# Kernel optimization log

Hardware: AMD Instinct MI355X
Metric: run time of the kernel (lower is better)

Reference implementation:

```python
import jax, jax.numpy as jnp
import numpy as np

# Constants matching init_kwargs
PC_MIN_X, PC_MIN_Y = -70.4, -40.0
VX, VY = 0.1, 0.1
RADII = (0.4, 0.8)
NSAMPLE = 16
EPS = 1e-5

B, K, N = 2, 2048, 16384
C_BEV, H_BEV, W_BEV = 256, 100, 176


def setup_inputs() -> dict:
    key = jax.random.key(0)
    ks = jax.random.split(key, 16)
    u = lambda k, s: jax.random.uniform(k, s, jnp.float32)
    kp = jnp.stack([
        u(ks[0], (B, K)) * 136.0 - 68.0,
        u(ks[1], (B, K)) * 76.0 - 38.0,
        u(ks[2], (B, K)) * 2.5 - 2.0,   # z in (-2.0, 0.5) -> kpt_mask all True
    ], axis=-1)
    pts = jnp.stack([
        u(ks[3], (B, N)) * 140.0 - 70.0,
        u(ks[4], (B, N)) * 80.0 - 40.0,
        u(ks[5], (B, N)) * 4.0 - 3.0,
    ], axis=-1)
    r = lambda k, s: jax.random.normal(k, s, jnp.float32)
    s01 = lambda k, s: r(k, s) * 0.1
    return {
        "keypoints": kp,
        "points_xyz": pts,
        "points_feat": r(ks[6], (B, N, 1)),
        "spatial_features": r(ks[7], (B, C_BEV, H_BEV, W_BEV)),
        "bev_stride": 8,
        "W0_s0": s01(ks[8], (16, 4)), "g0_s0": jnp.ones(16), "b0_s0": jnp.zeros(16),
        "W1_s0": s01(ks[9], (16, 16)), "g1_s0": jnp.ones(16), "b1_s0": jnp.zeros(16),
        "W0_s1": s01(ks[10], (16, 4)), "g0_s1": jnp.ones(16), "b0_s1": jnp.zeros(16),
        "W1_s1": s01(ks[11], (32, 16)), "g1_s1": jnp.ones(32), "b1_s1": jnp.zeros(32),
        "Wf": s01(ks[12], (128, 304)), "gf": jnp.ones(128), "bf": jnp.zeros(128),
    }


def _batchnorm(x, g, b, axes):
    m = x.mean(axes, keepdims=True)
    v = x.var(axes, keepdims=True)
    return (x - m) * jax.lax.rsqrt(v + EPS) * g + b


def _ball_group(dist2, xyz_b, feat_b, kp_b, radius, ns):
    """pcdet ball_query: first ns in-radius neighbors (index order), pad by first idx."""
    Kq, Np = dist2.shape
    within = dist2 < radius * radius                      # (K, N)
    order = jnp.cumsum(within, axis=1) - 1                # slot for each point
    valid = within & (order < ns)
    pos = jnp.where(valid, order, ns)                     # invalid -> overflow slot
    idx = jnp.zeros((Kq, ns + 1), jnp.int32)
    idx = idx.at[jnp.arange(Kq)[:, None], pos].set(
        jnp.broadcast_to(jnp.arange(Np, dtype=jnp.int32)[None, :], (Kq, Np)))
    idx = idx[:, :ns]
    cnt = within.sum(axis=1)
    slot_ok = jnp.arange(ns)[None, :] < cnt[:, None]
    idx = jnp.where(slot_ok, idx, idx[:, :1])             # replicate first found idx
    empty = cnt == 0
    grouped_xyz = xyz_b[idx] - kp_b[:, None, :]           # (K, ns, 3)
    grouped = jnp.concatenate([grouped_xyz, feat_b[idx]], axis=-1)  # (K, ns, 3+C)
    grouped = jnp.where(empty[:, None, None], 0.0, grouped)
    return grouped, empty


def _group_both_scales(xyz_b, feat_b, kp_b):
    # pairwise dist computed ONCE, shared across both radii
    dist2 = jnp.sum((kp_b[:, None, :] - xyz_b[None, :, :]) ** 2, axis=-1)  # (K, N)
    g0, e0 = _ball_group(dist2, xyz_b, feat_b, kp_b, RADII[0], NSAMPLE)
    g1, e1 = _ball_group(dist2, xyz_b, feat_b, kp_b, RADII[1], NSAMPLE)
    return g0, e0, g1, e1


def _shared_mlp_pool(grouped, empty, layers):
    x = grouped                                            # (B, K, ns, Cin)
    for (W, g, b) in layers:
        x = jnp.einsum('bknc,oc->bkno', x, W)
        x = _batchnorm(x, g, b, axes=(0, 1, 2))            # BN2d over stacked M*ns
        x = jax.nn.relu(x)
    pooled = x.max(axis=2)                                 # max over ns -> (B, K, Cout)
    return jnp.where(empty[:, :, None], 0.0, pooled)


def _bev_interp(bev, kp, stride):
    # bev: (B, C, H, W); kp: (B, K, 3)
    im = jnp.transpose(bev, (0, 2, 3, 1))                  # (B, H, W, C)
    x = (kp[..., 0] - PC_MIN_X) / VX / stride
    y = (kp[..., 1] - PC_MIN_Y) / VY / stride
    Hh, Ww = im.shape[1], im.shape[2]
    x0 = jnp.clip(jnp.floor(x).astype(jnp.int32), 0, Ww - 1)
    x1 = jnp.clip(jnp.floor(x).astype(jnp.int32) + 1, 0, Ww - 1)
    y0 = jnp.clip(jnp.floor(y).astype(jnp.int32), 0, Hh - 1)
    y1 = jnp.clip(jnp.floor(y).astype(jnp.int32) + 1, 0, Hh - 1)
    bidx = jnp.arange(im.shape[0])[:, None]
    Ia, Ib = im[bidx, y0, x0], im[bidx, y1, x0]
    Ic, Id = im[bidx, y0, x1], im[bidx, y1, x1]
    x0f, x1f = x0.astype(x.dtype), x1.astype(x.dtype)
    y0f, y1f = y0.astype(y.dtype), y1.astype(y.dtype)
    wa = ((x1f - x) * (y1f - y))[..., None]
    wb = ((x1f - x) * (y - y0f))[..., None]
    wc = ((x - x0f) * (y1f - y))[..., None]
    wd = ((x - x0f) * (y - y0f))[..., None]
    return Ia * wa + Ib * wb + Ic * wc + Id * wd           # (B, K, C)


def reference(keypoints, points_xyz, points_feat, spatial_features, bev_stride,
              W0_s0, g0_s0, b0_s0, W1_s0, g1_s0, b1_s0,
              W0_s1, g0_s1, b0_s1, W1_s1, g1_s1, b1_s1,
              Wf, gf, bf):
    Bb, Kk, _ = keypoints.shape
    # BEV bilinear interpolation
    bev_feat = _bev_interp(spatial_features, keypoints, bev_stride)  # (B, K, C_bev)
    # per-batch ball-query grouping (vmapped over batch)
    g0, e0, g1, e1 = jax.vmap(_group_both_scales)(points_xyz, points_feat, keypoints)
    p0 = _shared_mlp_pool(g0, e0, [(W0_s0, g0_s0, b0_s0), (W1_s0, g1_s0, b1_s0)])
    p1 = _shared_mlp_pool(g1, e1, [(W0_s1, g0_s1, b0_s1), (W1_s1, g1_s1, b1_s1)])
    pooled = jnp.concatenate([p0, p1], axis=-1)            # (B, K, 48)
    feats = jnp.concatenate([bev_feat, pooled], axis=-1).reshape(Bb * Kk, -1)  # (M, 304)
    # vsa_point_feature_fusion: Linear(no bias) + BN1d(train) + ReLU
    fused = feats @ Wf.T
    fused = jax.nn.relu(_batchnorm(fused, gf, bf, axes=(0,)))
    return fused                                           # (B*K, 128)
```

## Files before the change

kernel.cpp:

```cpp
#include <hip/hip_runtime.h>
#include <hip/hip_bf16.h>

#define NB    2
#define NK    2048
#define NPTS  16384
#define NBK   4096
#define MSAMP 65536.0f
#define MROW  4096.0f

__global__ __launch_bounds__(256) void mega_kernel(
    const float* __restrict__ kp, const float* __restrict__ pts,
    const float* __restrict__ pfeat, const float* __restrict__ bev,
    const int* __restrict__ stridep,
    float* __restrict__ g0buf, float* __restrict__ g1buf,
    int* __restrict__ cnt, float* __restrict__ part0,
    float* __restrict__ feats)
{
  __shared__ float sxyz[3072];
  __shared__ float sfeat[1024];
  __shared__ float slots[4][2][2][16][4];
  __shared__ float bred[4][28];
  const int t = threadIdx.x;

  if (blockIdx.x >= 512) {
    const int bk = blockIdx.x - 512;
    const int c  = t;
    const int b  = bk >> 11;
    const float st = (float)(*stridep);
    const float x = (kp[bk*3+0] - (-70.4f)) / 0.1f / st;
    const float y = (kp[bk*3+1] - (-40.0f)) / 0.1f / st;
    const int xf = (int)floorf(x), yf = (int)floorf(y);
    const int x0 = min(max(xf, 0), 175), x1 = min(max(xf + 1, 0), 175);
    const int y0 = min(max(yf, 0), 99),  y1 = min(max(yf + 1, 0), 99);
    const float x0f = (float)x0, x1f = (float)x1, y0f = (float)y0, y1f = (float)y1;
    const float wa = (x1f - x) * (y1f - y);
    const float wb = (x1f - x) * (y - y0f);
    const float wc = (x - x0f) * (y1f - y);
    const float wd = (x - x0f) * (y - y0f);
    const size_t base = ((size_t)b * 256 + c) * 17600;
    const float Ia = bev[base + y0 * 176 + x0];
    const float Ib = bev[base + y1 * 176 + x0];
    const float Ic = bev[base + y0 * 176 + x1];
    const float Id = bev[base + y1 * 176 + x1];
    feats[(size_t)bk * 304 + c] = Ia * wa + Ib * wb + Ic * wc + Id * wd;
    return;
  }

  const int gb = blockIdx.x;
  const int wave = t >> 6;
  const int lane = t & 63;
  const int bkA = gb * 8 + wave * 2;
  const int bkB = bkA + 1;
  const int b  = gb >> 8;
  const float kxA = kp[bkA*3+0], kyA = kp[bkA*3+1], kzA = kp[bkA*3+2];
  const float kxB = kp[bkB*3+0], kyB = kp[bkB*3+1], kzB = kp[bkB*3+2];
  const float* px = pts   + (size_t)b * NPTS * 3;
  const float* pf = pfeat + (size_t)b * NPTS;
  int c0A = 0, c1A = 0, c0B = 0, c1B = 0;
  bool done = false;
  const unsigned long long below = (1ull << lane) - 1ull;

  for (int tile = 0; tile < 16; tile++) {
    __syncthreads();
    {
      const float4* gsrc = (const float4*)(px + tile * 3072);
      float4* ldst = (float4*)sxyz;
      ldst[t]       = gsrc[t];
      ldst[t + 256] = gsrc[t + 256];
      ldst[t + 512] = gsrc[t + 512];
      #pragma unroll
      for (int i = 0; i < 4; i++) sfeat[t + i * 256] = pf[tile * 1024 + t + i * 256];
    }
    __syncthreads();
    if (!done) {
      for (int inner = 0; inner < 16; inner++) {
        const int pp = inner * 64 + lane;
        const float x = sxyz[pp*3+0];
        const float y = sxyz[pp*3+1];
        const float z = sxyz[pp*3+2];
        const float dxA = x - kxA, dyA = y - kyA, dzA = z - kzA;
        const float d2A = dxA*dxA + dyA*dyA + dzA*dzA;
        const float dxB = x - kxB, dyB = y - kyB, dzB = z - kzB;
        const float d2B = dxB*dxB + dyB*dyB + dzB*dzB;
        const bool w1a = d2A < 0.64f;
        const bool w1b = d2B < 0.64f;
        const unsigned long long m1a = __ballot(w1a);
        const unsigned long long m1b = __ballot(w1b);
        if (m1a | m1b) {
          const bool w0a = d2A < 0.16f;
          const bool w0b = d2B < 0.16f;
          const unsigned long long m0a = __ballot(w0a);
          const unsigned long long m0b = __ballot(w0b);
          const float f = sfeat[pp];
          {
            const int o0 = c0A + __popcll(m0a & below);
            if (w0a && o0 < 16) {
              slots[wave][0][0][o0][0] = dxA; slots[wave][0][0][o0][1] = dyA;
              slots[wave][0][0][o0][2] = dzA; slots[wave][0][0][o0][3] = f;
            }
            const int o1 = c1A + __popcll(m1a & below);
            if (w1a && o1 < 16) {
              slots[wave][0][1][o1][0] = dxA; slots[wave][0][1][o1][1] = dyA;
              slots[wave][0][1][o1][2] = dzA; slots[wave][0][1][o1][3] = f;
            }
            c0A += __popcll(m0a);
            c1A += __popcll(m1a);
          }
          {
            const int o0 = c0B + __popcll(m0b & below);
            if (w0b && o0 < 16) {
              slots[wave][1][0][o0][0] = dxB; slots[wave][1][0][o0][1] = dyB;
              slots[wave][1][0][o0][2] = dzB; slots[wave][1][0][o0][3] = f;
            }
            const int o1 = c1B + __popcll(m1b & below);
            if (w1b && o1 < 16) {
              slots[wave][1][1][o1][0] = dxB; slots[wave][1][1][o1][1] = dyB;
              slots[wave][1][1][o1][2] = dzB; slots[wave][1][1][o1][3] = f;
            }
            c0B += __popcll(m0b);
            c1B += __popcll(m1b);
          }
          if (c0A >= 16 && c0B >= 16) { done = true; break; }
        }
      }
    }
  }
  __syncthreads();

  {
    const int kpid = lane >> 5;
    const int s    = (lane >> 4) & 1;
    const int sl   = lane & 15;
    const int cs = kpid ? (s ? c1B : c0B) : (s ? c1A : c0A);
    if (cs == 0) {
      slots[wave][kpid][s][sl][0] = 0.f; slots[wave][kpid][s][sl][1] = 0.f;
      slots[wave][kpid][s][sl][2] = 0.f; slots[wave][kpid][s][sl][3] = 0.f;
    } else if (sl >= cs) {
      slots[wave][kpid][s][sl][0] = slots[wave][kpid][s][0][0];
      slots[wave][kpid][s][sl][1] = slots[wave][kpid][s][0][1];
      slots[wave][kpid][s][sl][2] = slots[wave][kpid][s][0][2];
      slots[wave][kpid][s][sl][3] = slots[wave][kpid][s][0][3];
    }
  }

  g0buf[(size_t)bkA * 64 + lane] = slots[wave][0][0][lane >> 2][lane & 3];
  g1buf[(size_t)bkA * 64 + lane] = slots[wave][0][1][lane >> 2][lane & 3];
  g0buf[(size_t)bkB * 64 + lane] = slots[wave][1][0][lane >> 2][lane & 3];
  g1buf[(size_t)bkB * 64 + lane] = slots[wave][1][1][lane >> 2][lane & 3];
  if (lane == 0) {
    cnt[bkA] = c0A; cnt[NBK + bkA] = c1A;
    cnt[bkB] = c0B; cnt[NBK + bkB] = c1B;
  }

  float v[14];
  {
    const int kpid = lane >> 5;
    const int s    = (lane >> 4) & 1;
    const int sl   = lane & 15;
    const float x0 = slots[wave][kpid][s][sl][0];
    const float x1 = slots[wave][kpid][s][sl][1];
    const float x2 = slots[wave][kpid][s][sl][2];
    const float x3 = slots[wave][kpid][s][sl][3];
    v[0] = x0; v[1] = x1; v[2] = x2; v[3] = x3;
    v[4] = x0*x0; v[5] = x0*x1; v[6]  = x0*x2; v[7]  = x0*x3;
    v[8] = x1*x1; v[9] = x1*x2; v[10] = x1*x3;
    v[11] = x2*x2; v[12] = x2*x3; v[13] = x3*x3;
  }
  #pragma unroll
  for (int d = 1; d < 16; d <<= 1) {
    #pragma unroll
    for (int i = 0; i < 14; i++) v[i] += __shfl_xor(v[i], d);
  }
  #pragma unroll
  for (int i = 0; i < 14; i++) v[i] += __shfl_xor(v[i], 32);
  if (lane == 0 || lane == 16) {
    float* dst = &bred[wave][(lane >> 4) * 14];
    #pragma unroll
    for (int i = 0; i < 14; i++) dst[i] = v[i];
  }
  __syncthreads();
  if (t < 28) {
    part0[gb * 28 + t] = bred[0][t] + bred[1][t] + bred[2][t] + bred[3][t];
  }
}

__device__ __forceinline__ void bn0_params(
    int t, const float* S0, const float* sW0a, const float* sW0b,
    const float* gm0s0, const float* bt0s0,
    const float* gm0s1, const float* bt0s1, float* sP)
{
  if (t < 32) {
    const int s = t >> 4, c = t & 15;
    const float* W  = s ? sW0b : sW0a;
    const float* G  = s ? gm0s1 : gm0s0;
    const float* Bt = s ? bt0s1 : bt0s0;
    const float* Sx = S0 + s * 14;
    const float w0 = W[c*4+0], w1 = W[c*4+1];
    const float w2 = W[c*4+2], w3 = W[c*4+3];
    const float inv = 1.0f / MSAMP;
    const float mean = (w0*Sx[0] + w1*Sx[1] + w2*Sx[2] + w3*Sx[3]) * inv;
    float e2 = w0*w0*Sx[4] + 2.f*w0*w1*Sx[5] + 2.f*w0*w2*Sx[6] + 2.f*w0*w3*Sx[7]
             + w1*w1*Sx[8] + 2.f*w1*w2*Sx[9] + 2.f*w1*w3*Sx[10]
             + w2*w2*Sx[11] + 2.f*w2*w3*Sx[12] + w3*w3*Sx[13];
    e2 *= inv;
    const float var = e2 - mean * mean;
    const float A = G[c] / sqrtf(var + 1e-5f);
    sP[s*32 + c]      = A;
    sP[s*32 + 16 + c] = Bt[c] - mean * A;
  }
}

__global__ __launch_bounds__(256) void stats1_kernel(
    const float* __restrict__ g0buf, const float* __restrict__ g1buf,
    const float* __restrict__ part0,
    const float* __restrict__ W0s0, const float* __restrict__ gm0s0, const float* __restrict__ bt0s0,
    const float* __restrict__ W0s1, const float* __restrict__ gm0s1, const float* __restrict__ bt0s1,
    const float* __restrict__ W1s0, const float* __restrict__ W1s1,
    float* __restrict__ part1)
{
  __shared__ float sW0a[64], sW0b[64], sW1a[256], sW1b[512], sP[64];
  __shared__ float tmp0[8][28], S0[28];
  __shared__ float red[16][96];
  const int t = threadIdx.x;
  if (t < 64) { sW0a[t] = W0s0[t]; sW0b[t] = W0s1[t]; }
  sW1a[t]       = W1s0[t];
  sW1b[t]       = W1s1[t];
  sW1b[t + 256] = W1s1[t + 256];
  for (int i = t; i < 16 * 96; i += 256) ((float*)red)[i] = 0.f;
  if (t < 224) {
    const int seg = t / 28, col = t % 28;
    float s = 0.f;
    for (int r = seg * 64; r < seg * 64 + 64; r++) s += part0[r * 28 + col];
    tmp0[seg][col] = s;
  }
  __syncthreads();
  if (t < 28) {
    float s = 0.f;
    #pragma unroll
    for (int g = 0; g < 8; g++) s += tmp0[g][t];
    S0[t] = s;
  }
  __syncthreads();
  bn0_params(t, S0, sW0a, sW0b, gm0s0, bt0s0, gm0s1, bt0s1, sP);
  __syncthreads();

  const int slot = blockIdx.x * 256 + t;
  const int wave = t >> 6, lane = t & 63;
  const int grp  = (wave << 2) | (lane >> 4);
  const bool leader = (lane & 15) == 0;

  float a1[16];
  {
    const float4 x = *(const float4*)(g0buf + (size_t)slot * 4);
    #pragma unroll
    for (int c = 0; c < 16; c++) {
      const float h = sW0a[c*4+0]*x.x + sW0a[c*4+1]*x.y + sW0a[c*4+2]*x.z + sW0a[c*4+3]*x.w;
      a1[c] = fmaxf(fmaf(sP[c], h, sP[16+c]), 0.f);
    }
    #pragma unroll
    for (int o = 0; o < 16; o++) {
      float h2 = 0.f;
      #pragma unroll
      for (int c = 0; c < 16; c++) h2 = fmaf(sW1a[o*16+c], a1[c], h2);
      float s = h2, q = h2 * h2;
      #pragma unroll
      for (int d = 1; d < 16; d <<= 1) { s += __shfl_xor(s, d); q += __shfl_xor(q, d); }
      if (leader) { red[grp][o] += s; red[grp][16+o] += q; }
    }
  }
  {
    const float4 x = *(const float4*)(g1buf + (size_t)slot * 4);
    #pragma unroll
    for (int c = 0; c < 16; c++) {
      const float h = sW0b[c*4+0]*x.x + sW0b[c*4+1]*x.y + sW0b[c*4+2]*x.z + sW0b[c*4+3]*x.w;
      a1[c] = fmaxf(fmaf(sP[32+c], h, sP[48+c]), 0.f);
    }
    #pragma unroll
    for (int o = 0; o < 32; o++) {
      float h2 = 0.f;
      #pragma unroll
      for (int c = 0; c < 16; c++) h2 = fmaf(sW1b[o*16+c], a1[c], h2);
      float s = h2, q = h2 * h2;
      #pragma unroll
      for (int d = 1; d < 16; d <<= 1) { s += __shfl_xor(s, d); q += __shfl_xor(q, d); }
      if (leader) { red[grp][32+o] += s; red[grp][64+o] += q; }
    }
  }
  __syncthreads();
  if (t < 96) {
    float s = 0.f;
    #pragma unroll
    for (int g = 0; g < 16; g++) s += red[g][t];
    part1[blockIdx.x * 96 + t] = s;
  }
}

__global__ __launch_bounds__(256) void poolgemm_kernel(
    const float* __restrict__ g0buf, const float* __restrict__ g1buf,
    const int* __restrict__ cnt,
    const float* __restrict__ part0, const float* __restrict__ part1,
    const float* __restrict__ W0s0, const float* __restrict__ gm0s0, const float* __restrict__ bt0s0,
    const float* __restrict__ W0s1, const float* __restrict__ gm0s1, const float* __restrict__ bt0s1,
    const float* __restrict__ W1s0, const float* __restrict__ gm1s0, const float* __restrict__ bt1s0,
    const float* __restrict__ W1s1, const float* __restrict__ gm1s1, const float* __restrict__ bt1s1,
    const float* __restrict__ feats, const float* __restrict__ Wf,
    float* __restrict__ fused, float* __restrict__ part2)
{
  __shared__ float sW0a[64], sW0b[64], sW1a[256], sW1b[512], sP[160];
  __shared__ float tmp0[8][28], S0[28];
  __shared__ float tmp1[2][96], S1[96];
  __shared__ __align__(16) float sF[16 * 304];
  const int t = threadIdx.x;
  const int bk0 = blockIdx.x * 16;

  for (int i = t; i < 4096; i += 256) {
    const int row = i >> 8, col = i & 255;
    sF[row * 304 + col] = feats[(size_t)(bk0 + row) * 304 + col];
  }
  if (t < 64)  { sW0a[t] = W0s0[t]; sW0b[t] = W0s1[t]; }
  sW1a[t]       = W1s0[t];
  sW1b[t]       = W1s1[t];
  sW1b[t + 256] = W1s1[t + 256];
  if (t < 224) {
    const int seg = t / 28, col = t % 28;
    float s = 0.f;
    for (int r = seg * 64; r < seg * 64 + 64; r++) s += part0[r * 28 + col];
    tmp0[seg][col] = s;
  }
  __syncthreads();
  if (t < 28) {
    float s = 0.f;
    #pragma unroll
    for (int g = 0; g < 8; g++) s += tmp0[g][t];
    S0[t] = s;
  }
  if (t >= 32 && t < 224) {
    const int tt = t - 32;
    const int seg = tt / 96, col = tt % 96;
    float s = 0.f;
    for (int r = seg * 128; r < seg * 128 + 128; r++) s += part1[r * 96 + col];
    tmp1[seg][col] = s;
  }
  __syncthreads();
  bn0_params(t, S0, sW0a, sW0b, gm0s0, bt0s0, gm0s1, bt0s1, sP);
  if (t >= 64 && t < 160) {
    const int c = t - 64;
    S1[c] = tmp1[0][c] + tmp1[1][c];
  }
  __syncthreads();
  if (t < 48) {
    float sum, sq, G, Bv; int oA, oB;
    if (t < 16) { sum = S1[t];    sq = S1[16+t]; G = gm1s0[t]; Bv = bt1s0[t]; oA = 64+t;  oB = 80+t; }
    else { const int c = t - 16; sum = S1[32+c]; sq = S1[64+c]; G = gm1s1[c]; Bv = bt1s1[c]; oA = 96+c; oB = 128+c; }
    const float mean = sum / MSAMP;
    const float var  = sq / MSAMP - mean * mean;
    const float A = G / sqrtf(var + 1e-5f);
    sP[oA] = A;
    sP[oB] = Bv - mean * A;
  }
  __syncthreads();

  {
    const int lkp = t >> 4, slot = t & 15;
    const int bk = bk0 + lkp;
    const size_t si = (size_t)bk * 16 + slot;
    float a1[16], a2s0[16], a2s1[32];
    {
      const float4 x = *(const float4*)(g0buf + si * 4);
      #pragma unroll
      for (int c = 0; c < 16; c++) {
        const float h = sW0a[c*4+0]*x.x + sW0a[c*4+1]*x.y + sW0a[c*4+2]*x.z + sW0a[c*4+3]*x.w;
        a1[c] = fmaxf(fmaf(sP[c], h, sP[16+c]), 0.f);
      }
      #pragma unroll
      for (int o = 0; o < 16; o++) {
        float h2 = 0.f;
        #pragma unroll
        for (int c = 0; c < 16; c++) h2 = fmaf(sW1a[o*16+c], a1[c], h2);
        a2s0[o] = fmaxf(fmaf(sP[64+o], h2, sP[80+o]), 0.f);
      }
    }
    {
      const float4 x = *(const float4*)(g1buf + si * 4);
      #pragma unroll
      for (int c = 0; c < 16; c++) {
        const float h = sW0b[c*4+0]*x.x + sW0b[c*4+1]*x.y + sW0b[c*4+2]*x.z + sW0b[c*4+3]*x.w;
        a1[c] = fmaxf(fmaf(sP[32+c], h, sP[48+c]), 0.f);
      }
      #pragma unroll
      for (int o = 0; o < 32; o++) {
        float h2 = 0.f;
        #pragma unroll
        for (int c = 0; c < 16; c++) h2 = fmaf(sW1b[o*16+c], a1[c], h2);
        a2s1[o] = fmaxf(fmaf(sP[96+o], h2, sP[128+o]), 0.f);
      }
    }
    #pragma unroll
    for (int d = 1; d < 16; d <<= 1) {
      #pragma unroll
      for (int o = 0; o < 16; o++) a2s0[o] = fmaxf(a2s0[o], __shfl_xor(a2s0[o], d));
      #pragma unroll
      for (int o = 0; o < 32; o++) a2s1[o] = fmaxf(a2s1[o], __shfl_xor(a2s1[o], d));
    }
    if (slot == 0) {
      const int c0 = cnt[bk], c1 = cnt[NBK + bk];
      float* outp = sF + lkp * 304 + 256;
      #pragma unroll
      for (int o = 0; o < 16; o++) outp[o] = c0 ? a2s0[o] : 0.f;
      #pragma unroll
      for (int o = 0; o < 32; o++) outp[16 + o] = c1 ? a2s1[o] : 0.f;
    }
  }
  __syncthreads();

  {
    const int c = t & 127;
    const int rbase = (t >> 7) * 8;
    float acc[8];
    #pragma unroll
    for (int r = 0; r < 8; r++) acc[r] = 0.f;
    const float* wrow = Wf + (size_t)c * 304;
    for (int j4 = 0; j4 < 76; j4++) {
      const float4 w = *(const float4*)(wrow + j4 * 4);
      #pragma unroll
      for (int r = 0; r < 8; r++) {
        const float4 f = *(const float4*)(sF + (rbase + r) * 304 + j4 * 4);
        acc[r] = fmaf(w.x, f.x, acc[r]);
        acc[r] = fmaf(w.y, f.y, acc[r]);
        acc[r] = fmaf(w.z, f.z, acc[r]);
        acc[r] = fmaf(w.w, f.w, acc[r]);
      }
    }
    float s = 0.f, q = 0.f;
    #pragma unroll
    for (int r = 0; r < 8; r++) {
      fused[(size_t)(bk0 + rbase + r) * 128 + c] = acc[r];
      s += acc[r];
      q = fmaf(acc[r], acc[r], q);
    }
    const int prow = blockIdx.x * 2 + (t >> 7);
    part2[prow * 256 + c]       = s;
    part2[prow * 256 + 128 + c] = q;
  }
}

__global__ __launch_bounds__(256) void out_kernel(
    const float* __restrict__ fused, const float* __restrict__ part2,
    const float* __restrict__ gf, const float* __restrict__ bfp,
    float* __restrict__ out)
{
  __shared__ float sA[128], sB[128];
  __shared__ float tmp[2][128];
  const int t = threadIdx.x;
  {
    const int c = t & 127, which = t >> 7;
    float s = 0.f;
    for (int r = 0; r < 512; r++) s += part2[r * 256 + which * 128 + c];
    tmp[which][c] = s;
  }
  __syncthreads();
  if (t < 128) {
    const float mean = tmp[0][t] / MROW;
    const float var  = tmp[1][t] / MROW - mean * mean;
    const float A = gf[t] / sqrtf(var + 1e-5f);
    sA[t] = A;
    sB[t] = bfp[t] - mean * A;
  }
  __syncthreads();
  #pragma unroll
  for (int k = 0; k < 4; k++) {
    const int f4 = blockIdx.x * 1024 + k * 256 + t;
    const int i = f4 * 4;
    const float4 v = *(const float4*)(fused + i);
    const int c = i & 127;
    float4 o;
    o.x = fmaxf(fmaf(v.x, sA[c+0], sB[c+0]), 0.f);
    o.y = fmaxf(fmaf(v.y, sA[c+1], sB[c+1]), 0.f);
    o.z = fmaxf(fmaf(v.z, sA[c+2], sB[c+2]), 0.f);
    o.w = fmaxf(fmaf(v.w, sA[c+3], sB[c+3]), 0.f);
    *(float4*)(out + i) = o;
  }
}

extern "C" void kernel_launch(void* const* d_in, const int* in_sizes, int n_in,
                              void* d_out, int out_size, void* d_ws, size_t ws_size,
                              hipStream_t stream)
{
  const float* kp    = (const float*)d_in[0];
  const float* pts   = (const float*)d_in[1];
  const float* pfeat = (const float*)d_in[2];
  const float* bev   = (const float*)d_in[3];
  const int*   strd  = (const int*)d_in[4];
  const float* W0s0  = (const float*)d_in[5];
  const float* g0s0  = (const float*)d_in[6];
  const float* b0s0  = (const float*)d_in[7];
  const float* W1s0  = (const float*)d_in[8];
  const float* g1s0  = (const float*)d_in[9];
  const float* b1s0  = (const float*)d_in[10];
  const float* W0s1  = (const float*)d_in[11];
  const float* g0s1  = (const float*)d_in[12];
  const float* b0s1  = (const float*)d_in[13];
  const float* W1s1  = (const float*)d_in[14];
  const float* g1s1  = (const float*)d_in[15];
  const float* b1s1  = (const float*)d_in[16];
  const float* Wf    = (const float*)d_in[17];
  const float* gf    = (const float*)d_in[18];
  const float* bfv   = (const float*)d_in[19];

  float* w      = (float*)d_ws;
  float* g0buf  = w;
  float* g1buf  = w + 262144;
  float* feats  = w + 524288;
  float* fused  = w + 1769472;
  float* part0  = w + 2293760;
  float* part1  = w + 2326528;
  float* part2  = w + 2351104;
  int*   cnt    = (int*)(w + 2482176);

  hipLaunchKernelGGL(mega_kernel,  dim3(4608), dim3(256), 0, stream,
                     kp, pts, pfeat, bev, strd, g0buf, g1buf, cnt, part0, feats);
  hipLaunchKernelGGL(stats1_kernel, dim3(256), dim3(256), 0, stream,
                     g0buf, g1buf, part0,
                     W0s0, g0s0, b0s0, W0s1, g0s1, b0s1, W1s0, W1s1, part1);
  hipLaunchKernelGGL(poolgemm_kernel, dim3(256), dim3(256), 0, stream,
                     g0buf, g1buf, cnt, part0, part1,
                     W0s0, g0s0, b0s0, W0s1, g0s1, b0s1,
                     W1s0, g1s0, b1s0, W1s1, g1s1, b1s1,
                     feats, Wf, fused, part2);
  hipLaunchKernelGGL(out_kernel,   dim3(128), dim3(256), 0, stream,
                     fused, part2, gf, bfv, (float*)d_out);
}
```

Measured before the change: 218.5 us.

## Transpose BEV map to channel-last and fuse bilinear gather into poolgemm

Instead of 4096 blocks each doing strided per-channel gathers from the channel-first BEV map, the mega kernel now transposes the whole BEV tensor to channel-last layout through an LDS tile. The bilinear interpolation then moves into poolgemm_kernel, where each thread reads a contiguous channel of the four neighbours and writes straight into shared memory, removing the intermediate feats buffer. The cost is a full read and write of the BEV tensor (about 36 MB) every call, in exchange for coalesced gathers and less global round-trip traffic.

```diff
diff --git a/kernel.cpp b/kernel.cpp
--- a/kernel.cpp
+++ b/kernel.cpp
@@ -11,44 +11,40 @@
 __global__ __launch_bounds__(256) void mega_kernel(
     const float* __restrict__ kp, const float* __restrict__ pts,
     const float* __restrict__ pfeat, const float* __restrict__ bev,
-    const int* __restrict__ stridep,
     float* __restrict__ g0buf, float* __restrict__ g1buf,
     int* __restrict__ cnt, float* __restrict__ part0,
-    float* __restrict__ feats)
+    float* __restrict__ bevT)
 {
   __shared__ float sxyz[3072];
   __shared__ float sfeat[1024];
   __shared__ float slots[4][2][2][16][4];
   __shared__ float bred[4][28];
+  __shared__ float ttile[64][65];
   const int t = threadIdx.x;
-
-  if (blockIdx.x >= 512) {
-    const int bk = blockIdx.x - 512;
-    const int c  = t;
-    const int b  = bk >> 11;
-    const float st = (float)(*stridep);
-    const float x = (kp[bk*3+0] - (-70.4f)) / 0.1f / st;
-    const float y = (kp[bk*3+1] - (-40.0f)) / 0.1f / st;
-    const int xf = (int)floorf(x), yf = (int)floorf(y);
-    const int x0 = min(max(xf, 0), 175), x1 = min(max(xf + 1, 0), 175);
-    const int y0 = min(max(yf, 0), 99),  y1 = min(max(yf + 1, 0), 99);
-    const float x0f = (float)x0, x1f = (float)x1, y0f = (float)y0, y1f = (float)y1;
-    const float wa = (x1f - x) * (y1f - y);
-    const float wb = (x1f - x) * (y - y0f);
-    const float wc = (x - x0f) * (y1f - y);
-    const float wd = (x - x0f) * (y - y0f);
-    const size_t base = ((size_t)b * 256 + c) * 17600;
-    const float Ia = bev[base + y0 * 176 + x0];
-    const float Ib = bev[base + y1 * 176 + x0];
-    const float Ic = bev[base + y0 * 176 + x1];
-    const float Id = bev[base + y1 * 176 + x1];
-    feats[(size_t)bk * 304 + c] = Ia * wa + Ib * wb + Ic * wc + Id * wd;
-    return;
-  }
-
-  const int gb = blockIdx.x;
   const int wave = t >> 6;
   const int lane = t & 63;
+
+  if (blockIdx.x >= 512) {
+    const int tb  = blockIdx.x - 512;
+    const int b   = tb / 1100;
+    const int rem = tb % 1100;
+    const int cg  = (rem / 275) * 64;
+    const int sp0 = (rem % 275) * 64;
+    #pragma unroll 4
+    for (int i = 0; i < 16; i++) {
+      const int c = cg + wave * 16 + i;
+      ttile[wave * 16 + i][lane] = bev[((size_t)(b * 256 + c)) * 17600 + sp0 + lane];
+    }
+    __syncthreads();
+    #pragma unroll 4
+    for (int i = 0; i < 16; i++) {
+      const int s = wave * 16 + i;
+      bevT[((size_t)b * 17600 + sp0 + s) * 256 + cg + lane] = ttile[lane][s];
+    }
+    return;
+  }
+
+  const int gb = blockIdx.x;
   const int bkA = gb * 8 + wave * 2;
   const int bkB = bkA + 1;
   const int b  = gb >> 8;
@@ -296,6 +292,8 @@
 }
 
 __global__ __launch_bounds__(256) void poolgemm_kernel(
+    const float* __restrict__ kp, const int* __restrict__ stridep,
+    const float* __restrict__ bevT,
     const float* __restrict__ g0buf, const float* __restrict__ g1buf,
     const int* __restrict__ cnt,
     const float* __restrict__ part0, const float* __restrict__ part1,
@@ -303,7 +301,7 @@
     const float* __restrict__ W0s1, const float* __restrict__ gm0s1, const float* __restrict__ bt0s1,
     const float* __restrict__ W1s0, const float* __restrict__ gm1s0, const float* __restrict__ bt1s0,
     const float* __restrict__ W1s1, const float* __restrict__ gm1s1, const float* __restrict__ bt1s1,
-    const float* __restrict__ feats, const float* __restrict__ Wf,
+    const float* __restrict__ Wf,
     float* __restrict__ fused, float* __restrict__ part2)
 {
   __shared__ float sW0a[64], sW0b[64], sW1a[256], sW1b[512], sP[160];
@@ -313,10 +311,30 @@
   const int t = threadIdx.x;
   const int bk0 = blockIdx.x * 16;
 
-  for (int i = t; i < 4096; i += 256) {
-    const int row = i >> 8, col = i & 255;
-    sF[row * 304 + col] = feats[(size_t)(bk0 + row) * 304 + col];
-  }
+  {
+    const float st = (float)(*stridep);
+    for (int r = 0; r < 16; r++) {
+      const int bk = bk0 + r;
+      const int b = bk >> 11;
+      const float x = (kp[bk*3+0] - (-70.4f)) / 0.1f / st;
+      const float y = (kp[bk*3+1] - (-40.0f)) / 0.1f / st;
+      const int xf = (int)floorf(x), yf = (int)floorf(y);
+      const int x0 = min(max(xf, 0), 175), x1 = min(max(xf + 1, 0), 175);
+      const int y0 = min(max(yf, 0), 99),  y1 = min(max(yf + 1, 0), 99);
+      const float x0f = (float)x0, x1f = (float)x1, y0f = (float)y0, y1f = (float)y1;
+      const float wa = (x1f - x) * (y1f - y);
+      const float wb = (x1f - x) * (y - y0f);
+      const float wc = (x - x0f) * (y1f - y);
+      const float wd = (x - x0f) * (y - y0f);
+      const size_t pb = (size_t)b * 17600 * 256;
+      const float Ia = bevT[pb + (size_t)(y0 * 176 + x0) * 256 + t];
+      const float Ib = bevT[pb + (size_t)(y1 * 176 + x0) * 256 + t];
+      const float Ic = bevT[pb + (size_t)(y0 * 176 + x1) * 256 + t];
+      const float Id = bevT[pb + (size_t)(y1 * 176 + x1) * 256 + t];
+      sF[r * 304 + t] = Ia * wa + Ib * wb + Ic * wc + Id * wd;
+    }
+  }
+
   if (t < 64)  { sW0a[t] = W0s0[t]; sW0b[t] = W0s1[t]; }
   sW1a[t]       = W1s0[t];
   sW1b[t]       = W1s1[t];
@@ -510,23 +528,23 @@
   float* w      = (float*)d_ws;
   float* g0buf  = w;
   float* g1buf  = w + 262144;
-  float* feats  = w + 524288;
-  float* fused  = w + 1769472;
-  float* part0  = w + 2293760;
-  float* part1  = w + 2326528;
-  float* part2  = w + 2351104;
-  int*   cnt    = (int*)(w + 2482176);
-
-  hipLaunchKernelGGL(mega_kernel,  dim3(4608), dim3(256), 0, stream,
-                     kp, pts, pfeat, bev, strd, g0buf, g1buf, cnt, part0, feats);
+  float* fused  = w + 524288;
+  float* part0  = w + 1048576;
+  float* part1  = w + 1081344;
+  float* part2  = w + 1105920;
+  int*   cnt    = (int*)(w + 1236992);
+  float* bevT   = w + 1245184;
+
+  hipLaunchKernelGGL(mega_kernel,  dim3(2712), dim3(256), 0, stream,
+                     kp, pts, pfeat, bev, g0buf, g1buf, cnt, part0, bevT);
   hipLaunchKernelGGL(stats1_kernel, dim3(256), dim3(256), 0, stream,
                      g0buf, g1buf, part0,
                      W0s0, g0s0, b0s0, W0s1, g0s1, b0s1, W1s0, W1s1, part1);
   hipLaunchKernelGGL(poolgemm_kernel, dim3(256), dim3(256), 0, stream,
-                     g0buf, g1buf, cnt, part0, part1,
+                     kp, strd, bevT, g0buf, g1buf, cnt, part0, part1,
                      W0s0, g0s0, b0s0, W0s1, g0s1, b0s1,
                      W1s0, g1s0, b1s0, W1s1, g1s1, b1s1,
-                     feats, Wf, fused, part2);
+                     Wf, fused, part2);
   hipLaunchKernelGGL(out_kernel,   dim3(128), dim3(256), 0, stream,
                      fused, part2, gf, bfv, (float*)d_out);
 }
```

After: 217.8 us. Within noise of the previous version (-0.3%).
